# Optimization experiments

Hardware: AMD Instinct MI355X
Metric: run time of the kernel (lower is better)

## Reference

```python
import jax, jax.numpy as jnp
import numpy as np

NUM_BASIS = 9  # ADVANCED_LIB in oikan: x, x^2, x^3, exp, log(|x|+1), sqrt(|x|), tanh, sin, abs


def _basis(x):
    # x: [B, Din] -> [B, Din, K] basis expansion matching ADVANCED_LIB
    ax = jnp.abs(x)
    return jnp.stack([
        x,
        x * x,
        x * x * x,
        jnp.exp(x),
        jnp.log(ax + 1.0),
        jnp.sqrt(ax),
        jnp.tanh(x),
        jnp.sin(x),
        ax,
    ], axis=-1)


def setup_inputs() -> dict:
    key = jax.random.key(0)
    k1, k2, k3 = jax.random.split(key, 3)
    B, Din, Dout, K = 4096, 128, 128, NUM_BASIS
    x = jax.random.normal(k1, (B, Din), dtype=jnp.float32)
    # per-edge basis weights (SymbolicEdge.weights ~ randn)
    W = jax.random.normal(k2, (Din, Dout, K), dtype=jnp.float32)
    # per-edge bias (initialized to zeros in SymbolicEdge)
    bias = jnp.zeros((Din, Dout), dtype=jnp.float32)
    # combination_weights ~ 0.1 * randn
    C = jax.random.normal(k3, (Din, Dout), dtype=jnp.float32) * 0.1
    return {"x": x, "W": W, "bias": bias, "C": C}


def reference(x, W, bias, C):
    feats = _basis(x)  # [B, Din, K]
    # edge_outputs[b, i, o] = sum_k feats[b,i,k] * W[i,o,k] + bias[i,o]
    edge = jnp.einsum('bik,iok->bio', feats, W) + bias  # [B, Din, Dout]
    # combined sum over input dim with combination weights
    return jnp.einsum('bio,io->bo', edge, C)  # [B, Dout]
```

## Files before the change

kernel.cpp:

```cpp
#include <hip/hip_runtime.h>
#include <math.h>


#define DIN   128
#define DOUT  128
#define NB    9
#define KK    (DIN * NB)
#define BATCH 4096
#define ROWS  16
#define APAD  8
#define ASTR  (KK + APAD)

typedef __bf16 bf16x8 __attribute__((ext_vector_type(8)));
typedef float  f32x4  __attribute__((ext_vector_type(4)));

__global__ __launch_bounds__(256) void fold_kernel(const float* __restrict__ W,
                                                   const float* __restrict__ bias,
                                                   const float* __restrict__ C,
                                                   __bf16* __restrict__ BT,
                                                   float* __restrict__ bterm) {
    const int idx = blockIdx.x * 256 + threadIdx.x;
    const int o = idx / KK;
    const int r = idx - o * KK;
    const int i = r / NB;
    const int k = r - i * NB;
    const float w = W[((size_t)i * DOUT + o) * NB + k];
    const float c = C[i * DOUT + o];
    BT[idx] = (__bf16)(w * c);

    if (blockIdx.x == 0 && threadIdx.x < DOUT) {
        const int oo = threadIdx.x;
        float s = 0.0f;
        for (int ii = 0; ii < DIN; ++ii)
            s += bias[ii * DOUT + oo] * C[ii * DOUT + oo];
        bterm[oo] = s;
    }
}

__global__ __launch_bounds__(512, 1) void fused_kernel(const float* __restrict__ x,
                                                       const __bf16* __restrict__ BT,
                                                       const float* __restrict__ bterm,
                                                       float* __restrict__ out) {
    __shared__ __bf16 As[ROWS * ASTR];
    const int t    = threadIdx.x;
    const int row0 = blockIdx.x * ROWS;

    for (int e = t; e < ROWS * DIN; e += 512) {
        const int r = e >> 7;
        const int i = e & 127;
        const float v  = x[(size_t)(row0 + r) * DIN + i];
        const float av = fabsf(v);
        float f[NB];
        f[0] = v;
        f[1] = v * v;
        f[2] = v * v * v;
        f[3] = __expf(v);
        f[4] = __logf(av + 1.0f);
        f[5] = __builtin_sqrtf(av);
        f[6] = tanhf(v);
        f[7] = __sinf(v);
        f[8] = av;
        __bf16* dst = &As[r * ASTR + i * NB];
        #pragma unroll
        for (int k = 0; k < NB; ++k) dst[k] = (__bf16)f[k];
    }
    __syncthreads();

    const int lane = t & 63;
    const int wave = t >> 6;
    const int m    = lane & 15;
    const int quad = lane >> 4;
    const int col0 = wave << 4;

    const __bf16* Ap = &As[m * ASTR + quad * 8];
    const __bf16* Bp = BT + (size_t)(col0 + m) * KK + quad * 8;

    f32x4 acc = {0.0f, 0.0f, 0.0f, 0.0f};

    #pragma unroll 6
    for (int kc = 0; kc < KK / 32; ++kc) {
        bf16x8 a = *(const bf16x8*)(Ap + kc * 32);
        bf16x8 b = *(const bf16x8*)(Bp + kc * 32);
        acc = __builtin_amdgcn_mfma_f32_16x16x32_bf16(a, b, acc, 0, 0, 0);
    }

    const float bt = bterm[col0 + m];
    float* op = out + (size_t)(row0 + quad * 4) * DOUT + col0 + m;
    #pragma unroll
    for (int r = 0; r < 4; ++r) op[(size_t)r * DOUT] = acc[r] + bt;
}

extern "C" void kernel_launch(void* const* d_in, const int* in_sizes, int n_in,
                              void* d_out, int out_size, void* d_ws, size_t ws_size,
                              hipStream_t stream) {
    const float* x    = (const float*)d_in[0];
    const float* W    = (const float*)d_in[1];
    const float* bias = (const float*)d_in[2];
    const float* C    = (const float*)d_in[3];
    float* out = (float*)d_out;

    char* ws = (char*)d_ws;
    __bf16* BT    = (__bf16*)ws;
    float*  bterm = (float*)(ws + (size_t)DOUT * KK * 2);

    fold_kernel<<<(DOUT * KK) / 256, 256, 0, stream>>>(W, bias, C, BT, bterm);
    fused_kernel<<<BATCH / ROWS, 512, 0, stream>>>(x, BT, bterm, out);
}
```

Baseline: 74.69 us.

## Pack bf16 pairs, fast tanh, and parallelize bias-term reduction in fold

The fold kernel now has each thread handle two input features for one output. It writes packed 32-bit bf16 pairs instead of single 16-bit stores and adds separate blocks that reduce the bias term with wave shuffles instead of one serial loop. The fused kernel's basis expansion processes two x values per thread using float2 loads and packed LDS stores. It also replaces tanhf with an exp/rcp formula. The aim is fewer, wider memory transactions and cheaper transcendental math, at a small accuracy cost from the approximate tanh.

Result: faster. 71.98 us (-3.6%).

```diff
diff --git a/kernel.cpp b/kernel.cpp
--- a/kernel.cpp
+++ b/kernel.cpp
@@ -13,27 +13,73 @@
 
 typedef __bf16 bf16x8 __attribute__((ext_vector_type(8)));
 typedef float  f32x4  __attribute__((ext_vector_type(4)));
+typedef unsigned int uint;
+
+__device__ __forceinline__ uint pack2(float lo, float hi) {
+    __bf16 l = (__bf16)lo, h = (__bf16)hi;
+    unsigned short ul, uh;
+    __builtin_memcpy(&ul, &l, 2);
+    __builtin_memcpy(&uh, &h, 2);
+    return (uint)ul | ((uint)uh << 16);
+}
+
+__device__ __forceinline__ void basis9(float v, float* f) {
+    const float av = fabsf(v);
+    f[0] = v;
+    f[1] = v * v;
+    f[2] = f[1] * v;
+    f[3] = __expf(v);
+    f[4] = __logf(av + 1.0f);
+    f[5] = __builtin_sqrtf(av);
+    const float e2 = __expf(-2.0f * av);
+    const float th = (1.0f - e2) * __builtin_amdgcn_rcpf(1.0f + e2);
+    f[6] = __builtin_copysignf(th, v);
+    f[7] = __sinf(v);
+    f[8] = av;
+}
 
 __global__ __launch_bounds__(256) void fold_kernel(const float* __restrict__ W,
                                                    const float* __restrict__ bias,
                                                    const float* __restrict__ C,
                                                    __bf16* __restrict__ BT,
                                                    float* __restrict__ bterm) {
-    const int idx = blockIdx.x * 256 + threadIdx.x;
-    const int o = idx / KK;
-    const int r = idx - o * KK;
-    const int i = r / NB;
-    const int k = r - i * NB;
-    const float w = W[((size_t)i * DOUT + o) * NB + k];
-    const float c = C[i * DOUT + o];
-    BT[idx] = (__bf16)(w * c);
+    const int b = blockIdx.x;
+    const int t = threadIdx.x;
 
-    if (blockIdx.x == 0 && threadIdx.x < DOUT) {
-        const int oo = threadIdx.x;
-        float s = 0.0f;
-        for (int ii = 0; ii < DIN; ++ii)
-            s += bias[ii * DOUT + oo] * C[ii * DOUT + oo];
-        bterm[oo] = s;
+    if (b < 32) {
+        const int e2 = b * 256 + t;
+        const int o  = e2 >> 6;
+        const int ip = e2 & 63;
+        const int i  = ip * 2;
+
+        const float c0 = C[i * DOUT + o];
+        const float c1 = C[(i + 1) * DOUT + o];
+        const float* w0 = W + ((size_t)i * DOUT + o) * NB;
+        const float* w1 = W + ((size_t)(i + 1) * DOUT + o) * NB;
+
+        float f[18];
+        #pragma unroll
+        for (int k = 0; k < NB; ++k) f[k]      = w0[k] * c0;
+        #pragma unroll
+        for (int k = 0; k < NB; ++k) f[NB + k] = w1[k] * c1;
+
+        uint* dst = (uint*)(BT + (size_t)o * KK + i * NB);
+        #pragma unroll
+        for (int j = 0; j < 9; ++j) dst[j] = pack2(f[2 * j], f[2 * j + 1]);
+    } else {
+        const int o = b - 32;
+        float p = 0.0f;
+        if (t < DIN) p = bias[t * DOUT + o] * C[t * DOUT + o];
+        p += __shfl_down(p, 32);
+        p += __shfl_down(p, 16);
+        p += __shfl_down(p, 8);
+        p += __shfl_down(p, 4);
+        p += __shfl_down(p, 2);
+        p += __shfl_down(p, 1);
+        __shared__ float red[4];
+        if ((t & 63) == 0) red[t >> 6] = p;
+        __syncthreads();
+        if (t == 0) bterm[o] = red[0] + red[1] + red[2] + red[3];
     }
 }
 
@@ -45,32 +91,35 @@
     const int t    = threadIdx.x;
     const int row0 = blockIdx.x * ROWS;
 
-    for (int e = t; e < ROWS * DIN; e += 512) {
-        const int r = e >> 7;
-        const int i = e & 127;
-        const float v  = x[(size_t)(row0 + r) * DIN + i];
-        const float av = fabsf(v);
-        float f[NB];
-        f[0] = v;
-        f[1] = v * v;
-        f[2] = v * v * v;
-        f[3] = __expf(v);
-        f[4] = __logf(av + 1.0f);
-        f[5] = __builtin_sqrtf(av);
-        f[6] = tanhf(v);
-        f[7] = __sinf(v);
-        f[8] = av;
-        __bf16* dst = &As[r * ASTR + i * NB];
-        #pragma unroll
-        for (int k = 0; k < NB; ++k) dst[k] = (__bf16)f[k];
-    }
-    __syncthreads();
-
     const int lane = t & 63;
     const int wave = t >> 6;
     const int m    = lane & 15;
     const int quad = lane >> 4;
     const int col0 = wave << 4;
+    const float bt = bterm[col0 + m];
+
+    #pragma unroll
+    for (int pp = 0; pp < 2; ++pp) {
+        const int p  = t + pp * 512;
+        const int r  = p >> 6;
+        const int ip = p & 63;
+        const int i  = ip * 2;
+        const float2 xv = *(const float2*)&x[(size_t)(row0 + r) * DIN + i];
+        float fa[9], fb[9];
+        basis9(xv.x, fa);
+        basis9(xv.y, fb);
+        uint* dst = (uint*)&As[r * ASTR + i * NB];
+        dst[0] = pack2(fa[0], fa[1]);
+        dst[1] = pack2(fa[2], fa[3]);
+        dst[2] = pack2(fa[4], fa[5]);
+        dst[3] = pack2(fa[6], fa[7]);
+        dst[4] = pack2(fa[8], fb[0]);
+        dst[5] = pack2(fb[1], fb[2]);
+        dst[6] = pack2(fb[3], fb[4]);
+        dst[7] = pack2(fb[5], fb[6]);
+        dst[8] = pack2(fb[7], fb[8]);
+    }
+    __syncthreads();
 
     const __bf16* Ap = &As[m * ASTR + quad * 8];
     const __bf16* Bp = BT + (size_t)(col0 + m) * KK + quad * 8;
@@ -84,7 +133,6 @@
         acc = __builtin_amdgcn_mfma_f32_16x16x32_bf16(a, b, acc, 0, 0, 0);
     }
 
-    const float bt = bterm[col0 + m];
     float* op = out + (size_t)(row0 + quad * 4) * DOUT + col0 + m;
     #pragma unroll
     for (int r = 0; r < 4; ++r) op[(size_t)r * DOUT] = acc[r] + bt;
@@ -103,6 +151,6 @@
     __bf16* BT    = (__bf16*)ws;
     float*  bterm = (float*)(ws + (size_t)DOUT * KK * 2);
 
-    fold_kernel<<<(DOUT * KK) / 256, 256, 0, stream>>>(W, bias, C, BT, bterm);
+    fold_kernel<<<160, 256, 0, stream>>>(W, bias, C, BT, bterm);
     fused_kernel<<<BATCH / ROWS, 512, 0, stream>>>(x, BT, bterm, out);
 }
```
